# Optimization experiments

Hardware: AMD Instinct MI355X
Metric: run time of the kernel (lower is better)

Reference implementation:

```python
import jax, jax.numpy as jnp
import numpy as np

B, N, D, DN, F, NUM_F, O, H = 8, 4096, 256, 128, 128, 1024, 8, 1024
EPS = 1e-5

def setup_inputs() -> dict:
    key = jax.random.key(0)
    ks = jax.random.split(key, 10)
    s = 0.02
    x = jax.random.normal(ks[0], (B, N, D), dtype=jnp.float32)
    ctx = jax.random.normal(ks[1], (B, DN), dtype=jnp.float32)
    idx = jax.random.randint(ks[2], (F,), 0, NUM_F, dtype=jnp.int64)
    cond_w = jax.random.normal(ks[3], (DN, 2 * D), dtype=jnp.float32) * s
    cond_b = jnp.zeros((2 * D,), dtype=jnp.float32)
    ffn_w_in = jax.random.normal(ks[4], (D, 2 * H), dtype=jnp.float32) * s
    ffn_b_in = jnp.zeros((2 * H,), dtype=jnp.float32)
    ffn_w_out = jax.random.normal(ks[5], (H, D), dtype=jnp.float32) * s
    ffn_b_out = jnp.zeros((D,), dtype=jnp.float32)
    emb = jax.random.normal(ks[6], (NUM_F, D * O), dtype=jnp.float32) * s
    return {"x": x, "ctx": ctx, "idx": idx, "cond_w": cond_w, "cond_b": cond_b,
            "ffn_w_in": ffn_w_in, "ffn_b_in": ffn_b_in,
            "ffn_w_out": ffn_w_out, "ffn_b_out": ffn_b_out, "emb": emb}

def reference(x, ctx, idx, cond_w, cond_b, ffn_w_in, ffn_b_in, ffn_w_out, ffn_b_out, emb):
    # Conditional LayerNorm: normalize over last dim, FiLM-style modulation from ctx
    mu = jnp.mean(x, axis=-1, keepdims=True)
    var = jnp.mean((x - mu) ** 2, axis=-1, keepdims=True)
    h = (x - mu) * jax.lax.rsqrt(var + EPS)                      # [B,N,D]
    ss = ctx @ cond_w + cond_b                                   # [B,2D]
    scale, shift = jnp.split(ss, 2, axis=-1)                     # [B,D] each
    h = h * (1.0 + scale[:, None, :]) + shift[:, None, :]
    # Gated FFN: in-proj -> (gelu(gate) * value) -> out-proj
    uv = h @ ffn_w_in + ffn_b_in                                 # [B,N,2H]
    u, v = jnp.split(uv, 2, axis=-1)
    y = (jax.nn.gelu(u) * v) @ ffn_w_out + ffn_b_out             # [B,N,D]
    # Embedding-generated per-feature output weights, then batched contraction
    w = emb[idx].reshape(F, D, O)                                # gather [F,D,O]
    out = jnp.einsum('bnd,fdo->bnfo', y, w)                      # [B,N,F,O]
    return out
```

## Files before the change

### kernel.cpp

```cpp
#include <hip/hip_runtime.h>
#include <cstdint>
#include <cstddef>

#define M_TOT 32768
#define D_    256
#define DN_   128
#define TWO_D 512
#define H_    1024
#define TWO_H 2048

typedef unsigned short ushort_t;
typedef __attribute__((ext_vector_type(8))) short bf16x8;
typedef __attribute__((ext_vector_type(4))) float f32x4;

__device__ __forceinline__ ushort_t f2bf(float f) {
  union { float f; uint32_t i; } v; v.f = f;
  uint32_t r = v.i + 0x7fffu + ((v.i >> 16) & 1u);
  return (ushort_t)(r >> 16);
}

__device__ __forceinline__ void async_ld16(const void* g, void* l) {
  __builtin_amdgcn_global_load_lds(
      (const __attribute__((address_space(1))) void*)g,
      (__attribute__((address_space(3))) void*)l, 16, 0, 0);
}

__global__ __launch_bounds__(256) void cond_ss_kernel(
    const float* __restrict__ ctx, const float* __restrict__ cond_w,
    const float* __restrict__ cond_b, float* __restrict__ ss) {
  int j = blockIdx.x * 256 + threadIdx.x;
  int b = j >> 9, col = j & 511;
  float acc = cond_b[col];
  for (int k = 0; k < DN_; ++k)
    acc += ctx[b * DN_ + k] * cond_w[k * TWO_D + col];
  ss[j] = acc;
}

__global__ __launch_bounds__(256) void transpose_f32_bf16_kernel(
    const float* __restrict__ in, ushort_t* __restrict__ out, int R, int C) {
  __shared__ float T[64 * 65];
  int ctiles = C >> 6;
  int bi = blockIdx.x / ctiles, bj = blockIdx.x % ctiles;
  int r0 = bi * 64, c0 = bj * 64;
  int tid = threadIdx.x;
#pragma unroll
  for (int it = 0; it < 16; ++it) {
    int idx = it * 256 + tid;
    int r = idx >> 6, c = idx & 63;
    T[r * 65 + c] = in[(size_t)(r0 + r) * C + c0 + c];
  }
  __syncthreads();
#pragma unroll
  for (int it = 0; it < 8; ++it) {
    int idx = it * 256 + tid;
    int a = idx >> 5;
    int b = (idx & 31) * 2;
    uint32_t pk = (uint32_t)f2bf(T[b * 65 + a]) |
                  ((uint32_t)f2bf(T[(b + 1) * 65 + a]) << 16);
    *(uint32_t*)&out[(size_t)(c0 + a) * R + r0 + b] = pk;
  }
}

__global__ __launch_bounds__(256) void gather_emb_kernel(
    const float* __restrict__ emb, const int* __restrict__ idx,
    ushort_t* __restrict__ W2T) {
  int f = blockIdx.x;
  bool looks64 = (idx[1] == 0) & (idx[3] == 0) & (idx[5] == 0) & (idx[7] == 0);
  int fi = looks64 ? idx[2 * f] : idx[f];
  const float* src = emb + (size_t)fi * 2048;
  int o = threadIdx.x >> 5, d0 = (threadIdx.x & 31) * 8;
  ushort_t buf[8];
#pragma unroll
  for (int k = 0; k < 8; ++k) buf[k] = f2bf(src[(d0 + k) * 8 + o]);
  *(bf16x8*)&W2T[(size_t)(f * 8 + o) * 256 + d0] = *(bf16x8*)buf;
}

__global__ __launch_bounds__(256) void ln_film_kernel(
    const float* __restrict__ x, const float* __restrict__ ss,
    ushort_t* __restrict__ h) {
  int row = blockIdx.x * 4 + (threadIdx.x >> 6);
  int lane = threadIdx.x & 63;
  int b = row >> 12;
  const float* xr = x + (size_t)row * D_;
  float4 pk = *(const float4*)(xr + lane * 4);
  float f0 = pk.x, f1 = pk.y, f2 = pk.z, f3 = pk.w;
  float s = f0 + f1 + f2 + f3;
  float q = f0 * f0 + f1 * f1 + f2 * f2 + f3 * f3;
#pragma unroll
  for (int off = 32; off > 0; off >>= 1) {
    s += __shfl_xor(s, off, 64);
    q += __shfl_xor(q, off, 64);
  }
  float mean = s * (1.0f / 256.0f);
  float var = q * (1.0f / 256.0f) - mean * mean;
  float rs = rsqrtf(var + 1e-5f);
  int d = lane * 4;
  const float* ssb = ss + b * TWO_D;
  float o0 = (f0 - mean) * rs * (1.0f + ssb[d + 0]) + ssb[256 + d + 0];
  float o1 = (f1 - mean) * rs * (1.0f + ssb[d + 1]) + ssb[256 + d + 1];
  float o2 = (f2 - mean) * rs * (1.0f + ssb[d + 2]) + ssb[256 + d + 2];
  float o3 = (f3 - mean) * rs * (1.0f + ssb[d + 3]) + ssb[256 + d + 3];
  uint2 st;
  st.x = (uint32_t)f2bf(o0) | ((uint32_t)f2bf(o1) << 16);
  st.y = (uint32_t)f2bf(o2) | ((uint32_t)f2bf(o3) << 16);
  *(uint2*)(h + (size_t)row * D_ + lane * 4) = st;
}

__global__ __launch_bounds__(256, 2) void ffn_fused_kernel(
    const ushort_t* __restrict__ h,
    const ushort_t* __restrict__ WinT,
    const float* __restrict__ bin,
    const ushort_t* __restrict__ WoutT,
    const float* __restrict__ bout,
    ushort_t* __restrict__ y) {
  __shared__ ushort_t S3[3][8192];
  __shared__ ushort_t Gs[64 * 72];
  __shared__ float Lbin[2048];
  const int tid = threadIdx.x, lane = tid & 63, wave = tid >> 6;
  const int wm = wave >> 1, wn = wave & 1;
  const int r = lane >> 2, q = lane & 3;
  const int qs = q ^ ((r >> 1) & 3);
  const int l15 = lane & 15, l4 = lane >> 4;
  const int m0 = blockIdx.x * 64;
  const int fragoff = l15 * 32 + (l4 ^ ((l15 >> 1) & 3)) * 8;

  const char* winb  = (const char*)WinT  + r * 512 + qs * 16;
  const char* woutb = (const char*)WoutT + r * 2048 + qs * 16;

  const ushort_t* hp = h + (size_t)(m0 + wm * 32 + l15) * 256 + l4 * 8;
  bf16x8 a_reg[2][8];
#pragma unroll
  for (int rt = 0; rt < 2; ++rt)
#pragma unroll
    for (int kc = 0; kc < 8; ++kc)
      a_reg[rt][kc] = *(const bf16x8*)(hp + rt * 4096 + kc * 32);

#pragma unroll
  for (int i = 0; i < 2; ++i)
    async_ld16((const char*)bin + (wave * 2 + i) * 1024 + lane * 16,
               (char*)Lbin + (wave * 2 + i) * 1024);

  auto stage_in = [&](ushort_t* dst, int jrow, int k0e) {
#pragma unroll
    for (int i = 0; i < 4; ++i) {
      int tt = i * 4 + wave;
      int vv = tt >> 3, t7 = tt & 7;
      int ks = t7 >> 2, cc = t7 & 3;
      async_ld16(winb + (size_t)vv * 524288 + jrow * 32768 + cc * 8192 +
                     k0e * 2 + ks * 64,
                 &dst[tt * 512]);
    }
  };
  auto stage_wout = [&](ushort_t* dst, int jrow, int s2) {
#pragma unroll
    for (int i = 0; i < 4; ++i) {
      int tt = i * 4 + wave;
      async_ld16(woutb + (size_t)tt * 32768 + jrow * 128 + s2 * 64,
                 &dst[tt * 512]);
    }
  };

  stage_in(S3[0], 0, 0);
  stage_in(S3[1], 0, 64);

  f32x4 yac[2][8] = {};

#define ENTRY4()                                        \
  asm volatile("s_waitcnt vmcnt(4)" ::: "memory");      \
  __builtin_amdgcn_s_barrier();                         \
  asm volatile("" ::: "memory");
#define ENTRY4L()                                                  \
  asm volatile("s_waitcnt vmcnt(4) lgkmcnt(0)" ::: "memory");      \
  __builtin_amdgcn_s_barrier();                                    \
  asm volatile("" ::: "memory");

#define MFMA_IN(buf, p_)                                                      \
  {                                                                           \
    const ushort_t* cur_ = (buf);                                             \
    __builtin_amdgcn_s_setprio(1);                                            \
    _Pragma("unroll")                                                         \
    for (int ks = 0; ks < 2; ++ks) {                                          \
      _Pragma("unroll")                                                       \
      for (int jj = 0; jj < 2; ++jj) {                                        \
        int tt = ks * 4 + wn * 2 + jj;                                        \
        bf16x8 bu = *(const bf16x8*)&cur_[tt * 512 + fragoff];                \
        bf16x8 bv = *(const bf16x8*)&cur_[(8 + tt) * 512 + fragoff];          \
        uac[0][jj] = __builtin_amdgcn_mfma_f32_16x16x32_bf16(a_reg[0][(p_)*2+ks], bu, uac[0][jj], 0, 0, 0); \
        uac[1][jj] = __builtin_amdgcn_mfma_f32_16x16x32_bf16(a_reg[1][(p_)*2+ks], bu, uac[1][jj], 0, 0, 0); \
        vac[0][jj] = __builtin_amdgcn_mfma_f32_16x16x32_bf16(a_reg[0][(p_)*2+ks], bv, vac[0][jj], 0, 0, 0); \
        vac[1][jj] = __builtin_amdgcn_mfma_f32_16x16x32_bf16(a_reg[1][(p_)*2+ks], bv, vac[1][jj], 0, 0, 0); \
      }                                                                       \
    }                                                                         \
    __builtin_amdgcn_s_setprio(0);                                            \
  }

#define MFMA_OUT(buf, s2_)                                                    \
  {                                                                           \
    const ushort_t* cur_ = (buf);                                             \
    bf16x8 gf0 = *(const bf16x8*)&Gs[(wm * 32 + l15) * 72 + (s2_) * 32 + l4 * 8];      \
    bf16x8 gf1 = *(const bf16x8*)&Gs[(wm * 32 + 16 + l15) * 72 + (s2_) * 32 + l4 * 8]; \
    __builtin_amdgcn_s_setprio(1);                                            \
    _Pragma("unroll")                                                         \
    for (int nt8 = 0; nt8 < 8; ++nt8) {                                       \
      bf16x8 bw = *(const bf16x8*)&cur_[(wn * 8 + nt8) * 512 + fragoff];      \
      yac[0][nt8] = __builtin_amdgcn_mfma_f32_16x16x32_bf16(gf0, bw, yac[0][nt8], 0, 0, 0); \
      yac[1][nt8] = __builtin_amdgcn_mfma_f32_16x16x32_bf16(gf1, bw, yac[1][nt8], 0, 0, 0); \
    }                                                                         \
    __builtin_amdgcn_s_setprio(0);                                            \
  }

  for (int j = 0; j < 16; ++j) {
    const int jn = (j + 1) & 15;
    f32x4 uac[2][2] = {}, vac[2][2] = {};

    ENTRY4(); stage_in(S3[2], j, 128);  MFMA_IN(S3[0], 0);
    ENTRY4(); stage_in(S3[0], j, 192);  MFMA_IN(S3[1], 1);
    ENTRY4(); stage_wout(S3[1], j, 0);  MFMA_IN(S3[2], 2);
    ENTRY4(); stage_wout(S3[2], j, 1);  MFMA_IN(S3[0], 3);

#pragma unroll
    for (int jj = 0; jj < 2; ++jj) {
      int gcol = wn * 32 + jj * 16 + l15;
      float bub = Lbin[j * 64 + gcol];
      float bvb = Lbin[1024 + j * 64 + gcol];
#pragma unroll
      for (int rt = 0; rt < 2; ++rt) {
#pragma unroll
        for (int rr = 0; rr < 4; ++rr) {
          float u = uac[rt][jj][rr] + bub;
          float v = vac[rt][jj][rr] + bvb;
          float t = 0.7978845608028654f * (u + 0.044715f * u * u * u);
          float e = __expf(2.0f * t);
          float th = 1.0f - 2.0f / (e + 1.0f);
          float gl = 0.5f * u * (1.0f + th);
          Gs[(wm * 32 + rt * 16 + l4 * 4 + rr) * 72 + gcol] = f2bf(gl * v);
        }
      }
    }

    ENTRY4L(); stage_in(S3[0], jn, 0);  MFMA_OUT(S3[1], 0);
    ENTRY4();  stage_in(S3[1], jn, 64); MFMA_OUT(S3[2], 1);
  }

  asm volatile("s_waitcnt vmcnt(0)" ::: "memory");
  __builtin_amdgcn_s_barrier();
  asm volatile("" ::: "memory");
  ushort_t* E = &S3[0][0];
#pragma unroll
  for (int hh = 0; hh < 2; ++hh) {
    if (wm == hh) {
#pragma unroll
      for (int nt8 = 0; nt8 < 8; ++nt8) {
        int col = wn * 128 + nt8 * 16 + l15;
        float bb = bout[col];
#pragma unroll
        for (int rt = 0; rt < 2; ++rt)
#pragma unroll
          for (int rr = 0; rr < 4; ++rr)
            E[(rt * 16 + l4 * 4 + rr) * 264 + col] = f2bf(yac[rt][nt8][rr] + bb);
      }
    }
    asm volatile("s_waitcnt lgkmcnt(0)" ::: "memory");
    __builtin_amdgcn_s_barrier();
    asm volatile("" ::: "memory");
#pragma unroll
    for (int it = 0; it < 4; ++it) {
      int id = it * 256 + tid;
      int rr = id >> 5, cc = id & 31;
      bf16x8 vv = *(const bf16x8*)&E[rr * 264 + cc * 8];
      *(bf16x8*)&y[(size_t)(m0 + hh * 32 + rr) * 256 + cc * 8] = vv;
    }
    if (hh == 0) {
      __builtin_amdgcn_s_barrier();
      asm volatile("" ::: "memory");
    }
  }
#undef ENTRY4
#undef ENTRY4L
#undef MFMA_IN
#undef MFMA_OUT
}

__global__ __launch_bounds__(256, 2) void gemm_out_kernel(
    const ushort_t* __restrict__ A, const ushort_t* __restrict__ BT,
    float* __restrict__ C) {
  __shared__ ushort_t As[128 * 64];
  __shared__ ushort_t Bs[128 * 64];
  __shared__ float Cs[64 * 132];
  const int tid = threadIdx.x, lane = tid & 63, wave = tid >> 6;
  const int wm = wave >> 1, wn = wave & 1;
  const int m0 = blockIdx.x * 128, n0 = blockIdx.y * 128;
  const int r = lane >> 2, q = lane & 3;
  const int qs = q ^ ((r >> 1) & 3);
  const int l15 = lane & 15, l4 = lane >> 4;
  const int fragoff = l15 * 32 + (l4 ^ ((l15 >> 1) & 3)) * 8;
  const int N = 1024, K = 256;
  f32x4 acc[4][4] = {};
  for (int k0 = 0; k0 < K; k0 += 64) {
    for (int t = wave; t < 16; t += 4) {
      int rt = t >> 1, ks = t & 1;
      async_ld16(A + (size_t)(m0 + rt * 16 + r) * K + k0 + ks * 32 + qs * 8, &As[t * 512]);
      async_ld16(BT + (size_t)(n0 + rt * 16 + r) * K + k0 + ks * 32 + qs * 8, &Bs[t * 512]);
    }
    __syncthreads();
#pragma unroll
    for (int ks = 0; ks < 2; ++ks) {
      bf16x8 a[4], b[4];
#pragma unroll
      for (int i = 0; i < 4; ++i)
        a[i] = *(const bf16x8*)&As[((wm * 4 + i) * 2 + ks) * 512 + fragoff];
#pragma unroll
      for (int jt = 0; jt < 4; ++jt)
        b[jt] = *(const bf16x8*)&Bs[((wn * 4 + jt) * 2 + ks) * 512 + fragoff];
#pragma unroll
      for (int i = 0; i < 4; ++i)
#pragma unroll
        for (int jt = 0; jt < 4; ++jt)
          acc[i][jt] = __builtin_amdgcn_mfma_f32_16x16x32_bf16(a[i], b[jt], acc[i][jt], 0, 0, 0);
    }
    __syncthreads();
  }
#pragma unroll
  for (int p = 0; p < 2; ++p) {
    __syncthreads();
    if (wm == p) {
#pragma unroll
      for (int jt = 0; jt < 4; ++jt) {
        int col = wn * 64 + jt * 16 + l15;
#pragma unroll
        for (int i = 0; i < 4; ++i) {
          int rl = i * 16 + (l4 << 2);
#pragma unroll
          for (int rr = 0; rr < 4; ++rr)
            Cs[(rl + rr) * 132 + col] = acc[i][jt][rr];
        }
      }
    }
    __syncthreads();
#pragma unroll
    for (int it = 0; it < 8; ++it) {
      int t = it * 256 + tid;
      int rr = t >> 5, c = (t & 31) * 4;
      float4 v = *(const float4*)&Cs[rr * 132 + c];
      *(float4*)&C[(size_t)(m0 + p * 64 + rr) * N + n0 + c] = v;
    }
  }
}

extern "C" void kernel_launch(void* const* d_in, const int* in_sizes, int n_in,
                              void* d_out, int out_size, void* d_ws, size_t ws_size,
                              hipStream_t stream) {
  const float* x      = (const float*)d_in[0];
  const float* ctx    = (const float*)d_in[1];
  const int*   idx    = (const int*)d_in[2];
  const float* cond_w = (const float*)d_in[3];
  const float* cond_b = (const float*)d_in[4];
  const float* w_in   = (const float*)d_in[5];
  const float* b_in   = (const float*)d_in[6];
  const float* w_out  = (const float*)d_in[7];
  const float* b_out  = (const float*)d_in[8];
  const float* emb    = (const float*)d_in[9];

  char* w = (char*)d_ws;
  float* ss = (float*)w;           w += (size_t)8 * TWO_D * 4;
  ushort_t* h = (ushort_t*)w;      w += (size_t)M_TOT * D_ * 2;
  ushort_t* y = (ushort_t*)w;      w += (size_t)M_TOT * D_ * 2;
  ushort_t* WinT = (ushort_t*)w;   w += (size_t)TWO_H * D_ * 2;
  ushort_t* WoutT = (ushort_t*)w;  w += (size_t)D_ * H_ * 2;
  ushort_t* W2T = (ushort_t*)w;    w += (size_t)H_ * D_ * 2;

  cond_ss_kernel<<<16, 256, 0, stream>>>(ctx, cond_w, cond_b, ss);
  transpose_f32_bf16_kernel<<<(D_ / 64) * (TWO_H / 64), 256, 0, stream>>>(w_in, WinT, D_, TWO_H);
  transpose_f32_bf16_kernel<<<(H_ / 64) * (D_ / 64), 256, 0, stream>>>(w_out, WoutT, H_, D_);
  gather_emb_kernel<<<128, 256, 0, stream>>>(emb, idx, W2T);
  ln_film_kernel<<<M_TOT / 4, 256, 0, stream>>>(x, ss, h);
  ffn_fused_kernel<<<M_TOT / 64, 256, 0, stream>>>(h, WinT, b_in, WoutT, b_out, y);
  gemm_out_kernel<<<dim3(M_TOT / 128, H_ / 128), 256, 0, stream>>>(y, W2T, (float*)d_out);
}
```

Baseline: 289.4 us.

## Double FFN block rows to 512 threads and double-buffer output GEMM

The fused FFN kernel now runs 8 waves over 128 rows per block. Each weight tile staged into shared memory is reused by twice as many rows, and per-thread load counts and wait thresholds are halved to match. The output GEMM gains a double-buffered async K pipeline and writes fp32 results straight from registers instead of through a shared-memory transpose. The risks are lower occupancy for the larger FFN block and uncoalesced direct stores in the output GEMM.

```diff
diff --git a/kernel.cpp b/kernel.cpp
--- a/kernel.cpp
+++ b/kernel.cpp
@@ -106,7 +106,7 @@
   *(uint2*)(h + (size_t)row * D_ + lane * 4) = st;
 }
 
-__global__ __launch_bounds__(256, 2) void ffn_fused_kernel(
+__global__ __launch_bounds__(512, 2) void ffn_fused_kernel(
     const ushort_t* __restrict__ h,
     const ushort_t* __restrict__ WinT,
     const float* __restrict__ bin,
@@ -114,14 +114,14 @@
     const float* __restrict__ bout,
     ushort_t* __restrict__ y) {
   __shared__ ushort_t S3[3][8192];
-  __shared__ ushort_t Gs[64 * 72];
+  __shared__ ushort_t Gs[128 * 72];
   __shared__ float Lbin[2048];
   const int tid = threadIdx.x, lane = tid & 63, wave = tid >> 6;
   const int wm = wave >> 1, wn = wave & 1;
   const int r = lane >> 2, q = lane & 3;
   const int qs = q ^ ((r >> 1) & 3);
   const int l15 = lane & 15, l4 = lane >> 4;
-  const int m0 = blockIdx.x * 64;
+  const int m0 = blockIdx.x * 128;
   const int fragoff = l15 * 32 + (l4 ^ ((l15 >> 1) & 3)) * 8;
 
   const char* winb  = (const char*)WinT  + r * 512 + qs * 16;
@@ -135,15 +135,13 @@
     for (int kc = 0; kc < 8; ++kc)
       a_reg[rt][kc] = *(const bf16x8*)(hp + rt * 4096 + kc * 32);
 
-#pragma unroll
-  for (int i = 0; i < 2; ++i)
-    async_ld16((const char*)bin + (wave * 2 + i) * 1024 + lane * 16,
-               (char*)Lbin + (wave * 2 + i) * 1024);
+  async_ld16((const char*)bin + wave * 1024 + lane * 16,
+             (char*)Lbin + wave * 1024);
 
   auto stage_in = [&](ushort_t* dst, int jrow, int k0e) {
 #pragma unroll
-    for (int i = 0; i < 4; ++i) {
-      int tt = i * 4 + wave;
+    for (int i = 0; i < 2; ++i) {
+      int tt = i * 8 + wave;
       int vv = tt >> 3, t7 = tt & 7;
       int ks = t7 >> 2, cc = t7 & 3;
       async_ld16(winb + (size_t)vv * 524288 + jrow * 32768 + cc * 8192 +
@@ -153,8 +151,8 @@
   };
   auto stage_wout = [&](ushort_t* dst, int jrow, int s2) {
 #pragma unroll
-    for (int i = 0; i < 4; ++i) {
-      int tt = i * 4 + wave;
+    for (int i = 0; i < 2; ++i) {
+      int tt = i * 8 + wave;
       async_ld16(woutb + (size_t)tt * 32768 + jrow * 128 + s2 * 64,
                  &dst[tt * 512]);
     }
@@ -165,12 +163,12 @@
 
   f32x4 yac[2][8] = {};
 
-#define ENTRY4()                                        \
-  asm volatile("s_waitcnt vmcnt(4)" ::: "memory");      \
+#define ENTRY2()                                        \
+  asm volatile("s_waitcnt vmcnt(2)" ::: "memory");      \
   __builtin_amdgcn_s_barrier();                         \
   asm volatile("" ::: "memory");
-#define ENTRY4L()                                                  \
-  asm volatile("s_waitcnt vmcnt(4) lgkmcnt(0)" ::: "memory");      \
+#define ENTRY2L()                                                  \
+  asm volatile("s_waitcnt vmcnt(2) lgkmcnt(0)" ::: "memory");      \
   __builtin_amdgcn_s_barrier();                                    \
   asm volatile("" ::: "memory");
 
@@ -213,10 +211,10 @@
     const int jn = (j + 1) & 15;
     f32x4 uac[2][2] = {}, vac[2][2] = {};
 
-    ENTRY4(); stage_in(S3[2], j, 128);  MFMA_IN(S3[0], 0);
-    ENTRY4(); stage_in(S3[0], j, 192);  MFMA_IN(S3[1], 1);
-    ENTRY4(); stage_wout(S3[1], j, 0);  MFMA_IN(S3[2], 2);
-    ENTRY4(); stage_wout(S3[2], j, 1);  MFMA_IN(S3[0], 3);
+    ENTRY2(); stage_in(S3[2], j, 128);  MFMA_IN(S3[0], 0);
+    ENTRY2(); stage_in(S3[0], j, 192);  MFMA_IN(S3[1], 1);
+    ENTRY2(); stage_wout(S3[1], j, 0);  MFMA_IN(S3[2], 2);
+    ENTRY2(); stage_wout(S3[2], j, 1);  MFMA_IN(S3[0], 3);
 
 #pragma unroll
     for (int jj = 0; jj < 2; ++jj) {
@@ -238,8 +236,8 @@
       }
     }
 
-    ENTRY4L(); stage_in(S3[0], jn, 0);  MFMA_OUT(S3[1], 0);
-    ENTRY4();  stage_in(S3[1], jn, 64); MFMA_OUT(S3[2], 1);
+    ENTRY2L(); stage_in(S3[0], jn, 0);  MFMA_OUT(S3[1], 0);
+    ENTRY2();  stage_in(S3[1], jn, 64); MFMA_OUT(S3[2], 1);
   }
 
   asm volatile("s_waitcnt vmcnt(0)" ::: "memory");
@@ -248,7 +246,8 @@
   ushort_t* E = &S3[0][0];
 #pragma unroll
   for (int hh = 0; hh < 2; ++hh) {
-    if (wm == hh) {
+    if ((wm >> 1) == hh) {
+      int er0 = (wm & 1) * 32;
 #pragma unroll
       for (int nt8 = 0; nt8 < 8; ++nt8) {
         int col = wn * 128 + nt8 * 16 + l15;
@@ -257,7 +256,7 @@
         for (int rt = 0; rt < 2; ++rt)
 #pragma unroll
           for (int rr = 0; rr < 4; ++rr)
-            E[(rt * 16 + l4 * 4 + rr) * 264 + col] = f2bf(yac[rt][nt8][rr] + bb);
+            E[(er0 + rt * 16 + l4 * 4 + rr) * 264 + col] = f2bf(yac[rt][nt8][rr] + bb);
       }
     }
     asm volatile("s_waitcnt lgkmcnt(0)" ::: "memory");
@@ -265,18 +264,18 @@
     asm volatile("" ::: "memory");
 #pragma unroll
     for (int it = 0; it < 4; ++it) {
-      int id = it * 256 + tid;
+      int id = it * 512 + tid;
       int rr = id >> 5, cc = id & 31;
       bf16x8 vv = *(const bf16x8*)&E[rr * 264 + cc * 8];
-      *(bf16x8*)&y[(size_t)(m0 + hh * 32 + rr) * 256 + cc * 8] = vv;
+      *(bf16x8*)&y[(size_t)(m0 + hh * 64 + rr) * 256 + cc * 8] = vv;
     }
     if (hh == 0) {
       __builtin_amdgcn_s_barrier();
       asm volatile("" ::: "memory");
     }
   }
-#undef ENTRY4
-#undef ENTRY4L
+#undef ENTRY2
+#undef ENTRY2L
 #undef MFMA_IN
 #undef MFMA_OUT
 }
@@ -284,9 +283,7 @@
 __global__ __launch_bounds__(256, 2) void gemm_out_kernel(
     const ushort_t* __restrict__ A, const ushort_t* __restrict__ BT,
     float* __restrict__ C) {
-  __shared__ ushort_t As[128 * 64];
-  __shared__ ushort_t Bs[128 * 64];
-  __shared__ float Cs[64 * 132];
+  __shared__ ushort_t SB[2][16384];
   const int tid = threadIdx.x, lane = tid & 63, wave = tid >> 6;
   const int wm = wave >> 1, wn = wave & 1;
   const int m0 = blockIdx.x * 128, n0 = blockIdx.y * 128;
@@ -295,54 +292,59 @@
   const int l15 = lane & 15, l4 = lane >> 4;
   const int fragoff = l15 * 32 + (l4 ^ ((l15 >> 1) & 3)) * 8;
   const int N = 1024, K = 256;
+
+  auto stage = [&](ushort_t* dst, int k0) {
+#pragma unroll
+    for (int i = 0; i < 4; ++i) {
+      int t = i * 4 + wave;
+      int rt = t >> 1, ks = t & 1;
+      async_ld16(A + (size_t)(m0 + rt * 16 + r) * K + k0 + ks * 32 + qs * 8, &dst[t * 512]);
+      async_ld16(BT + (size_t)(n0 + rt * 16 + r) * K + k0 + ks * 32 + qs * 8, &dst[(16 + t) * 512]);
+    }
+  };
+
   f32x4 acc[4][4] = {};
-  for (int k0 = 0; k0 < K; k0 += 64) {
-    for (int t = wave; t < 16; t += 4) {
-      int rt = t >> 1, ks = t & 1;
-      async_ld16(A + (size_t)(m0 + rt * 16 + r) * K + k0 + ks * 32 + qs * 8, &As[t * 512]);
-      async_ld16(BT + (size_t)(n0 + rt * 16 + r) * K + k0 + ks * 32 + qs * 8, &Bs[t * 512]);
-    }
-    __syncthreads();
+  stage(SB[0], 0);
+#pragma unroll
+  for (int ki = 0; ki < 4; ++ki) {
+    __builtin_amdgcn_s_barrier();
+    asm volatile("" ::: "memory");
+    if (ki < 3) {
+      stage(SB[(ki + 1) & 1], (ki + 1) * 64);
+      asm volatile("s_waitcnt vmcnt(8)" ::: "memory");
+    } else {
+      asm volatile("s_waitcnt vmcnt(0)" ::: "memory");
+    }
+    __builtin_amdgcn_s_barrier();
+    asm volatile("" ::: "memory");
+    const ushort_t* cur = SB[ki & 1];
+    __builtin_amdgcn_s_setprio(1);
 #pragma unroll
     for (int ks = 0; ks < 2; ++ks) {
       bf16x8 a[4], b[4];
 #pragma unroll
       for (int i = 0; i < 4; ++i)
-        a[i] = *(const bf16x8*)&As[((wm * 4 + i) * 2 + ks) * 512 + fragoff];
+        a[i] = *(const bf16x8*)&cur[((wm * 4 + i) * 2 + ks) * 512 + fragoff];
 #pragma unroll
       for (int jt = 0; jt < 4; ++jt)
-        b[jt] = *(const bf16x8*)&Bs[((wn * 4 + jt) * 2 + ks) * 512 + fragoff];
+        b[jt] = *(const bf16x8*)&cur[(16 + (wn * 4 + jt) * 2 + ks) * 512 + fragoff];
 #pragma unroll
       for (int i = 0; i < 4; ++i)
 #pragma unroll
         for (int jt = 0; jt < 4; ++jt)
           acc[i][jt] = __builtin_amdgcn_mfma_f32_16x16x32_bf16(a[i], b[jt], acc[i][jt], 0, 0, 0);
     }
-    __syncthreads();
-  }
-#pragma unroll
-  for (int p = 0; p < 2; ++p) {
-    __syncthreads();
-    if (wm == p) {
-#pragma unroll
-      for (int jt = 0; jt < 4; ++jt) {
-        int col = wn * 64 + jt * 16 + l15;
-#pragma unroll
-        for (int i = 0; i < 4; ++i) {
-          int rl = i * 16 + (l4 << 2);
-#pragma unroll
-          for (int rr = 0; rr < 4; ++rr)
-            Cs[(rl + rr) * 132 + col] = acc[i][jt][rr];
-        }
-      }
-    }
-    __syncthreads();
-#pragma unroll
-    for (int it = 0; it < 8; ++it) {
-      int t = it * 256 + tid;
-      int rr = t >> 5, c = (t & 31) * 4;
-      float4 v = *(const float4*)&Cs[rr * 132 + c];
-      *(float4*)&C[(size_t)(m0 + p * 64 + rr) * N + n0 + c] = v;
+    __builtin_amdgcn_s_setprio(0);
+  }
+#pragma unroll
+  for (int jt = 0; jt < 4; ++jt) {
+    int col = n0 + wn * 64 + jt * 16 + l15;
+#pragma unroll
+    for (int i = 0; i < 4; ++i) {
+      int row = m0 + wm * 64 + i * 16 + l4 * 4;
+#pragma unroll
+      for (int rr = 0; rr < 4; ++rr)
+        C[(size_t)(row + rr) * N + col] = acc[i][jt][rr];
     }
   }
 }
@@ -374,6 +376,6 @@
   transpose_f32_bf16_kernel<<<(H_ / 64) * (D_ / 64), 256, 0, stream>>>(w_out, WoutT, H_, D_);
   gather_emb_kernel<<<128, 256, 0, stream>>>(emb, idx, W2T);
   ln_film_kernel<<<M_TOT / 4, 256, 0, stream>>>(x, ss, h);
-  ffn_fused_kernel<<<M_TOT / 64, 256, 0, stream>>>(h, WinT, b_in, WoutT, b_out, y);
+  ffn_fused_kernel<<<M_TOT / 128, 512, 0, stream>>>(h, WinT, b_in, WoutT, b_out, y);
   gemm_out_kernel<<<dim3(M_TOT / 128, H_ / 128), 256, 0, stream>>>(y, W2T, (float*)d_out);
 }
```

Result: no change. 292.9 us (+1.2%).
